# Kernel tuning notes

Measured on AMD Instinct MI355X. Metric: run time of the kernel, lower is better.

## Reference

```python
import jax, jax.numpy as jnp
import numpy as np

EMBED = 1024
HEADS = 16
HEAD_DIM = EMBED // HEADS


def setup_inputs() -> dict:
    key = jax.random.key(0)
    ks = jax.random.split(key, 9)
    s = 1.0 / np.sqrt(EMBED)
    inp = {
        "x": jax.random.normal(ks[0], (2, 2048, EMBED), dtype=jnp.float32),
        "wq": jax.random.uniform(ks[1], (EMBED, EMBED), jnp.float32, -s, s),
        "bq": jax.random.uniform(ks[2], (EMBED,), jnp.float32, -s, s),
        "wk": jax.random.uniform(ks[3], (EMBED, EMBED), jnp.float32, -s, s),
        "bk": jax.random.uniform(ks[4], (EMBED,), jnp.float32, -s, s),
        "wv": jax.random.uniform(ks[5], (EMBED, EMBED), jnp.float32, -s, s),
        "bv": jax.random.uniform(ks[6], (EMBED,), jnp.float32, -s, s),
        "wo": jax.random.uniform(ks[7], (EMBED, EMBED), jnp.float32, -s, s),
        "bo": jax.random.uniform(ks[8], (EMBED,), jnp.float32, -s, s),
    }
    return inp


def reference(x, wq, bq, wk, bk, wv, bv, wo, bo):
    B, S, E = x.shape
    H, D = HEADS, HEAD_DIM
    # projections (torch Linear: y = x @ W.T + b; here weights stored as [E, E] applied as x @ W.T)
    q = (x @ wq.T + bq).reshape(B, S, H, D).transpose(0, 2, 1, 3)  # [B,H,S,D]
    k = (x @ wk.T + bk).reshape(B, S, H, D).transpose(0, 2, 1, 3)
    v = (x @ wv.T + bv).reshape(B, S, H, D).transpose(0, 2, 1, 3)
    scores = jnp.einsum("bhqd,bhkd->bhqk", q, k) / jnp.sqrt(jnp.asarray(D, x.dtype))
    attn = jax.nn.softmax(scores, axis=-1)  # dropout is identity in eval / p=0
    ctx = jnp.einsum("bhqk,bhkd->bhqd", attn, v)
    ctx = ctx.transpose(0, 2, 1, 3).reshape(B, S, E)
    return ctx @ wo.T + bo
```

## Files before the change

kernel.cpp:

```cpp
#include <hip/hip_runtime.h>
#include <hip/hip_bf16.h>

#define EMBED 1024
#define HEADS 16
#define HDIM  64
#define BATCH 2
#define SEQ   2048
#define MTOT  (BATCH*SEQ)

typedef __attribute__((ext_vector_type(8))) short bf16x8;
typedef __attribute__((ext_vector_type(4))) short bf16x4;
typedef __attribute__((ext_vector_type(4))) float f32x4;
typedef __attribute__((ext_vector_type(8))) unsigned short u16x8;
typedef __attribute__((ext_vector_type(2))) unsigned u32x2;
typedef __attribute__((ext_vector_type(4))) unsigned u32x4;

__device__ __forceinline__ unsigned pack2(float lo, float hi) {
    __hip_bfloat162 h = __float22bfloat162_rn(make_float2(lo, hi));
    unsigned u;
    __builtin_memcpy(&u, &h, sizeof(u));
    return u;
}
__device__ __forceinline__ unsigned short f2bf(float f) {
    __hip_bfloat16 h = __float2bfloat16(f);
    unsigned short u;
    __builtin_memcpy(&u, &h, sizeof(u));
    return u;
}
__device__ __forceinline__ u16x8 cvt8(float4 a, float4 b) {
    u32x4 r;
    r[0] = pack2(a.x, a.y);
    r[1] = pack2(a.z, a.w);
    r[2] = pack2(b.x, b.y);
    r[3] = pack2(b.z, b.w);
    return __builtin_bit_cast(u16x8, r);
}

__device__ __forceinline__ f32x4 mfma16(bf16x4 a, bf16x4 b, f32x4 c) {
#if __has_builtin(__builtin_amdgcn_mfma_f32_16x16x16bf16_1k)
    return __builtin_amdgcn_mfma_f32_16x16x16bf16_1k(a, b, c, 0, 0, 0);
#else
    f32x4 d;
    asm volatile("v_mfma_f32_16x16x16_bf16 %0, %1, %2, %3"
                 : "=v"(d) : "v"(a), "v"(b), "v"(c));
    return d;
#endif
}

__global__ __launch_bounds__(256, 2) void qkv_proj(
    const float* __restrict__ x,
    const float* __restrict__ wq, const float* __restrict__ bq,
    const float* __restrict__ wk, const float* __restrict__ bk,
    const float* __restrict__ wv, const float* __restrict__ bv,
    unsigned short* __restrict__ qo,
    unsigned short* __restrict__ ko,
    unsigned short* __restrict__ vto)
{
    const int which = blockIdx.z;
    const float* __restrict__ w    = (which == 0) ? wq : (which == 1) ? wk : wv;
    const float* __restrict__ bias = (which == 0) ? bq : (which == 1) ? bk : bv;
    const float kscale = (which == 1) ? 0.18033688f : 1.0f;

    const int m0 = blockIdx.x * 128;
    const int n0 = blockIdx.y * 128;

    __shared__ unsigned short a_lds[128][40];
    __shared__ unsigned short b_lds[128][40];

    const int tid  = threadIdx.x;
    const int lane = tid & 63;
    const int wid  = tid >> 6;
    const int wr   = wid >> 1, wc = wid & 1;
    const int lq   = lane & 15;
    const int lg   = lane >> 4;

    f32x4 acc[4][4] = {};

    const int srow = tid >> 2;
    const int scol = (tid & 3) * 8;

    for (int k0 = 0; k0 < EMBED; k0 += 32) {
        #pragma unroll
        for (int p = 0; p < 2; ++p) {
            const int r = srow + p * 64;
            const float4* sa = (const float4*)(x + (size_t)(m0 + r) * EMBED + k0 + scol);
            *(u16x8*)&a_lds[r][scol] = cvt8(sa[0], sa[1]);
            const float4* sb = (const float4*)(w + (size_t)(n0 + r) * EMBED + k0 + scol);
            *(u16x8*)&b_lds[r][scol] = cvt8(sb[0], sb[1]);
        }
        __syncthreads();
        bf16x8 af[4], bfr[4];
        #pragma unroll
        for (int i = 0; i < 4; ++i)
            af[i] = *(const bf16x8*)&a_lds[wr*64 + i*16 + lq][lg*8];
        #pragma unroll
        for (int j = 0; j < 4; ++j)
            bfr[j] = *(const bf16x8*)&b_lds[wc*64 + j*16 + lq][lg*8];
        #pragma unroll
        for (int i = 0; i < 4; ++i)
            #pragma unroll
            for (int j = 0; j < 4; ++j)
                acc[i][j] = __builtin_amdgcn_mfma_f32_16x16x32_bf16(af[i], bfr[j], acc[i][j], 0, 0, 0);
        __syncthreads();
    }

    #pragma unroll
    for (int j = 0; j < 4; ++j) {
        const int nn = n0 + wc*64 + j*16 + lq;
        const float bsv = bias[nn];
        const int h = nn >> 6, d = nn & (HDIM-1);
        #pragma unroll
        for (int i = 0; i < 4; ++i) {
            const int mmb = m0 + wr*64 + i*16 + lg*4;
            const int b = mmb >> 11;
            const int s = mmb & (SEQ-1);
            const size_t bh = (size_t)(b*HEADS + h);
            if (which == 2) {
                u32x2 ov;
                ov[0] = pack2(acc[i][j][0] + bsv, acc[i][j][1] + bsv);
                ov[1] = pack2(acc[i][j][2] + bsv, acc[i][j][3] + bsv);
                *(u32x2*)&vto[(bh*HDIM + d)*SEQ + s] = ov;
            } else {
                unsigned short* o = (which == 0) ? qo : ko;
                #pragma unroll
                for (int r = 0; r < 4; ++r)
                    o[(bh*SEQ + (s + r))*HDIM + d] = f2bf((acc[i][j][r] + bsv) * kscale);
            }
        }
    }
}

__global__ __launch_bounds__(256, 4) void attn(
    const unsigned short* __restrict__ q,
    const unsigned short* __restrict__ k,
    const unsigned short* __restrict__ vt,
    unsigned short* __restrict__ ctx)
{
    __shared__ __align__(16) unsigned char sm[2 * 16384];

    const int bid   = blockIdx.x;
    const int xcd   = bid & 7;
    const int local = bid >> 3;
    const int bh    = xcd * 4 + (local >> 5);
    const int q0    = (local & 31) * 64;
    const int b     = bh >> 4;
    const int h     = bh & (HEADS - 1);
    const int tid   = threadIdx.x;
    const int wv    = tid >> 6;
    const int lane  = tid & 63;
    const int lq = lane & 15, lg = lane >> 4;

    const unsigned short* qb = q  + (size_t)bh * SEQ * HDIM;
    const unsigned short* kb = k  + (size_t)bh * SEQ * HDIM;
    const unsigned short* vb = vt + (size_t)bh * HDIM * SEQ;

    const int swz    = (lq & 7) << 4;
    const int kread0 = lq*128 + ((lg*16)      ^ swz);
    const int kread1 = lq*128 + ((lg*16 + 64) ^ swz);
    int vroff[4];
    #pragma unroll
    for (int sub = 0; sub < 4; ++sub)
        vroff[sub] = lq*128 + ((sub*32 + lg*8) ^ swz);

    const int wrow = tid >> 3;
    const int woff = wrow*128 + ((((tid & 7) * 16)) ^ ((wrow & 7) << 4));

    const int scol = (tid & 7) * 8;
    const unsigned short* kp = kb + (size_t)wrow * HDIM + scol;
    const unsigned short* vp = vb + (size_t)wrow * SEQ + scol;

    bf16x8 qf[2];
    #pragma unroll
    for (int hh = 0; hh < 2; ++hh)
        qf[hh] = *(const bf16x8*)(qb + (size_t)(q0 + wv*16 + lq) * HDIM + hh*32 + lg*8);

    f32x4 o[4] = {};
    float lr = 0.f;

    u16x8 kr0, kr1, vr0, vr1;

#define LOADT() do {                                                           \
    kr0 = *(const u16x8*)(kp);                                                 \
    kr1 = *(const u16x8*)(kp + 32*HDIM);                                       \
    vr0 = *(const u16x8*)(vp);                                                 \
    vr1 = *(const u16x8*)(vp + 32*SEQ);                                        \
} while (0)

#define WRITET(BF) do {                                                        \
    *(u16x8*)(sm + (BF)*16384 +         woff) = kr0;                           \
    *(u16x8*)(sm + (BF)*16384 +  4096 + woff) = kr1;                           \
    *(u16x8*)(sm + (BF)*16384 +  8192 + woff) = vr0;                           \
    *(u16x8*)(sm + (BF)*16384 + 12288 + woff) = vr1;                           \
} while (0)

#define COMPUTE(BF) do {                                                       \
    f32x4 s_[4];                                                               \
    _Pragma("unroll")                                                          \
    for (int sub = 0; sub < 4; ++sub) {                                        \
        bf16x8 k0 = *(const bf16x8*)(sm + (BF)*16384 + sub*2048 + kread0);     \
        bf16x8 k1 = *(const bf16x8*)(sm + (BF)*16384 + sub*2048 + kread1);     \
        f32x4 z = {};                                                          \
        z = __builtin_amdgcn_mfma_f32_16x16x32_bf16(k0, qf[0], z, 0, 0, 0);    \
        z = __builtin_amdgcn_mfma_f32_16x16x32_bf16(k1, qf[1], z, 0, 0, 0);    \
        s_[sub] = z;                                                           \
    }                                                                          \
    bf16x4 pf[4];                                                              \
    float psum = 0.f;                                                          \
    _Pragma("unroll")                                                          \
    for (int sub = 0; sub < 4; ++sub) {                                        \
        f32x4 pv;                                                              \
        _Pragma("unroll")                                                      \
        for (int r = 0; r < 4; ++r) pv[r] = exp2f(s_[sub][r]);                 \
        psum += (pv[0] + pv[1]) + (pv[2] + pv[3]);                             \
        u32x2 pk;                                                              \
        pk[0] = pack2(pv[0], pv[1]);                                           \
        pk[1] = pack2(pv[2], pv[3]);                                           \
        pf[sub] = __builtin_bit_cast(bf16x4, pk);                              \
    }                                                                          \
    lr += psum;                                                                \
    _Pragma("unroll")                                                          \
    for (int sub = 0; sub < 4; ++sub) {                                        \
        _Pragma("unroll")                                                      \
        for (int i = 0; i < 4; ++i) {                                          \
            bf16x4 vfr = *(const bf16x4*)(sm + (BF)*16384 + 8192 + i*2048      \
                                          + vroff[sub]);                       \
            o[i] = mfma16(vfr, pf[sub], o[i]);                                 \
        }                                                                      \
    }                                                                          \
} while (0)

    LOADT();
    WRITET(0);
    __syncthreads();
    kp += 64 * HDIM;
    vp += 64;

    for (int t2 = 0; t2 < 16; ++t2) {
        {
            const int t = 2 * t2;
            if (t < 31) LOADT();
            COMPUTE(0);
            if (t < 31) {
                WRITET(1);
                __syncthreads();
                kp += 64 * HDIM;
                vp += 64;
            }
        }
        {
            const int t = 2 * t2 + 1;
            if (t < 31) LOADT();
            COMPUTE(1);
            if (t < 31) {
                WRITET(0);
                __syncthreads();
                kp += 64 * HDIM;
                vp += 64;
            }
        }
    }

#undef LOADT
#undef WRITET
#undef COMPUTE

    float lm = lr + __shfl_xor(lr, 16);
    lm += __shfl_xor(lm, 32);
    const float inv = 1.0f / lm;
    unsigned short* cb = ctx + ((size_t)(b*SEQ + q0 + wv*16 + lq)) * EMBED + h*HDIM;
    #pragma unroll
    for (int i = 0; i < 4; ++i) {
        u32x2 ov;
        ov[0] = pack2(o[i][0] * inv, o[i][1] * inv);
        ov[1] = pack2(o[i][2] * inv, o[i][3] * inv);
        *(u32x2*)(cb + i*16 + lg*4) = ov;
    }
}

__global__ __launch_bounds__(256, 2) void out_proj(
    const unsigned short* __restrict__ ctx,
    const float* __restrict__ wo, const float* __restrict__ bo,
    float* __restrict__ out)
{
    const int m0 = blockIdx.x * 128;
    const int n0 = blockIdx.y * 128;

    __shared__ unsigned short a_lds[128][40];
    __shared__ unsigned short b_lds[128][40];

    const int tid  = threadIdx.x;
    const int lane = tid & 63;
    const int wid  = tid >> 6;
    const int wr   = wid >> 1, wc = wid & 1;
    const int lq   = lane & 15;
    const int lg   = lane >> 4;

    f32x4 acc[4][4] = {};

    const int srow = tid >> 2;
    const int scol = (tid & 3) * 8;

    for (int k0 = 0; k0 < EMBED; k0 += 32) {
        #pragma unroll
        for (int p = 0; p < 2; ++p) {
            const int r = srow + p * 64;
            *(u16x8*)&a_lds[r][scol] =
                *(const u16x8*)(ctx + (size_t)(m0 + r) * EMBED + k0 + scol);
            const float4* sb = (const float4*)(wo + (size_t)(n0 + r) * EMBED + k0 + scol);
            *(u16x8*)&b_lds[r][scol] = cvt8(sb[0], sb[1]);
        }
        __syncthreads();
        bf16x8 af[4], bfr[4];
        #pragma unroll
        for (int i = 0; i < 4; ++i)
            af[i] = *(const bf16x8*)&a_lds[wr*64 + i*16 + lq][lg*8];
        #pragma unroll
        for (int j = 0; j < 4; ++j)
            bfr[j] = *(const bf16x8*)&b_lds[wc*64 + j*16 + lq][lg*8];
        #pragma unroll
        for (int i = 0; i < 4; ++i)
            #pragma unroll
            for (int j = 0; j < 4; ++j)
                acc[i][j] = __builtin_amdgcn_mfma_f32_16x16x32_bf16(af[i], bfr[j], acc[i][j], 0, 0, 0);
        __syncthreads();
    }

    #pragma unroll
    for (int j = 0; j < 4; ++j) {
        const int nn = n0 + wc*64 + j*16 + lq;
        const float bsv = bo[nn];
        #pragma unroll
        for (int i = 0; i < 4; ++i) {
            const int mm = m0 + wr*64 + i*16 + lg*4;
            #pragma unroll
            for (int r = 0; r < 4; ++r)
                out[(size_t)(mm + r) * EMBED + nn] = acc[i][j][r] + bsv;
        }
    }
}

extern "C" void kernel_launch(void* const* d_in, const int* in_sizes, int n_in,
                              void* d_out, int out_size, void* d_ws, size_t ws_size,
                              hipStream_t stream) {
    const float* x  = (const float*)d_in[0];
    const float* wq = (const float*)d_in[1];
    const float* bq = (const float*)d_in[2];
    const float* wk = (const float*)d_in[3];
    const float* bk = (const float*)d_in[4];
    const float* wv = (const float*)d_in[5];
    const float* bv = (const float*)d_in[6];
    const float* wo = (const float*)d_in[7];
    const float* bo = (const float*)d_in[8];
    float* out = (float*)d_out;

    const size_t NELEM = (size_t)MTOT * EMBED;
    unsigned short* q_ws   = (unsigned short*)d_ws;
    unsigned short* k_ws   = q_ws  + NELEM;
    unsigned short* vt_ws  = k_ws  + NELEM;
    unsigned short* ctx_ws = vt_ws + NELEM;

    qkv_proj<<<dim3(MTOT/128, EMBED/128, 3), 256, 0, stream>>>(
        x, wq, bq, wk, bk, wv, bv, q_ws, k_ws, vt_ws);
    attn<<<dim3(SEQ/64 * BATCH*HEADS), 256, 0, stream>>>(q_ws, k_ws, vt_ws, ctx_ws);
    out_proj<<<dim3(MTOT/128, EMBED/128), 256, 0, stream>>>(ctx_ws, wo, bo, out);
}
```

Baseline: 150.9 us.

## Load V fragments directly from global memory into registers, bypassing LDS

The attention kernel now has each wave read its V^T MFMA operand fragments straight from global memory into registers at the start of each tile, instead of staging V through shared memory. This halves the LDS footprint and removes the V LDS stores and reads. In exchange, every wave in the block re-reads the same V data from global memory or cache with narrow 8-byte loads. The loads are issued right before the compute that consumes them, so their latency may be exposed and register pressure rises.

```diff
diff --git a/kernel.cpp b/kernel.cpp
--- a/kernel.cpp
+++ b/kernel.cpp
@@ -136,7 +136,7 @@
     const unsigned short* __restrict__ vt,
     unsigned short* __restrict__ ctx)
 {
-    __shared__ __align__(16) unsigned char sm[2 * 16384];
+    __shared__ __align__(16) unsigned char sm[2 * 8192];
 
     const int bid   = blockIdx.x;
     const int xcd   = bid & 7;
@@ -157,17 +157,17 @@
     const int swz    = (lq & 7) << 4;
     const int kread0 = lq*128 + ((lg*16)      ^ swz);
     const int kread1 = lq*128 + ((lg*16 + 64) ^ swz);
-    int vroff[4];
-    #pragma unroll
-    for (int sub = 0; sub < 4; ++sub)
-        vroff[sub] = lq*128 + ((sub*32 + lg*8) ^ swz);
 
     const int wrow = tid >> 3;
     const int woff = wrow*128 + ((((tid & 7) * 16)) ^ ((wrow & 7) << 4));
 
     const int scol = (tid & 7) * 8;
     const unsigned short* kp = kb + (size_t)wrow * HDIM + scol;
-    const unsigned short* vp = vb + (size_t)wrow * SEQ + scol;
+
+    const unsigned short* vbp[4];
+    #pragma unroll
+    for (int i = 0; i < 4; ++i)
+        vbp[i] = vb + (size_t)(i*16 + lq) * SEQ + lg*4;
 
     bf16x8 qf[2];
     #pragma unroll
@@ -177,28 +177,36 @@
     f32x4 o[4] = {};
     float lr = 0.f;
 
-    u16x8 kr0, kr1, vr0, vr1;
+    u16x8 kr0, kr1;
+    bf16x4 vf[4][4];
 
 #define LOADT() do {                                                           \
     kr0 = *(const u16x8*)(kp);                                                 \
     kr1 = *(const u16x8*)(kp + 32*HDIM);                                       \
-    vr0 = *(const u16x8*)(vp);                                                 \
-    vr1 = *(const u16x8*)(vp + 32*SEQ);                                        \
 } while (0)
 
 #define WRITET(BF) do {                                                        \
-    *(u16x8*)(sm + (BF)*16384 +         woff) = kr0;                           \
-    *(u16x8*)(sm + (BF)*16384 +  4096 + woff) = kr1;                           \
-    *(u16x8*)(sm + (BF)*16384 +  8192 + woff) = vr0;                           \
-    *(u16x8*)(sm + (BF)*16384 + 12288 + woff) = vr1;                           \
+    *(u16x8*)(sm + (BF)*8192 +        woff) = kr0;                             \
+    *(u16x8*)(sm + (BF)*8192 + 4096 + woff) = kr1;                             \
+} while (0)
+
+#define VISSUE() do {                                                          \
+    _Pragma("unroll")                                                          \
+    for (int i = 0; i < 4; ++i) {                                              \
+        vf[0][i] = *(const bf16x4*)(vbp[i]);                                   \
+        vf[1][i] = *(const bf16x4*)(vbp[i] + 16);                              \
+        vf[2][i] = *(const bf16x4*)(vbp[i] + 32);                              \
+        vf[3][i] = *(const bf16x4*)(vbp[i] + 48);                              \
+        vbp[i] += 64;                                                          \
+    }                                                                          \
 } while (0)
 
 #define COMPUTE(BF) do {                                                       \
     f32x4 s_[4];                                                               \
     _Pragma("unroll")                                                          \
     for (int sub = 0; sub < 4; ++sub) {                                        \
-        bf16x8 k0 = *(const bf16x8*)(sm + (BF)*16384 + sub*2048 + kread0);     \
-        bf16x8 k1 = *(const bf16x8*)(sm + (BF)*16384 + sub*2048 + kread1);     \
+        bf16x8 k0 = *(const bf16x8*)(sm + (BF)*8192 + sub*2048 + kread0);      \
+        bf16x8 k1 = *(const bf16x8*)(sm + (BF)*8192 + sub*2048 + kread1);      \
         f32x4 z = {};                                                          \
         z = __builtin_amdgcn_mfma_f32_16x16x32_bf16(k0, qf[0], z, 0, 0, 0);    \
         z = __builtin_amdgcn_mfma_f32_16x16x32_bf16(k1, qf[1], z, 0, 0, 0);    \
@@ -221,11 +229,8 @@
     _Pragma("unroll")                                                          \
     for (int sub = 0; sub < 4; ++sub) {                                        \
         _Pragma("unroll")                                                      \
-        for (int i = 0; i < 4; ++i) {                                          \
-            bf16x4 vfr = *(const bf16x4*)(sm + (BF)*16384 + 8192 + i*2048      \
-                                          + vroff[sub]);                       \
-            o[i] = mfma16(vfr, pf[sub], o[i]);                                 \
-        }                                                                      \
+        for (int i = 0; i < 4; ++i)                                            \
+            o[i] = mfma16(vf[sub][i], pf[sub], o[i]);                          \
     }                                                                          \
 } while (0)
 
@@ -233,35 +238,35 @@
     WRITET(0);
     __syncthreads();
     kp += 64 * HDIM;
-    vp += 64;
 
     for (int t2 = 0; t2 < 16; ++t2) {
         {
             const int t = 2 * t2;
+            VISSUE();
             if (t < 31) LOADT();
             COMPUTE(0);
             if (t < 31) {
                 WRITET(1);
                 __syncthreads();
                 kp += 64 * HDIM;
-                vp += 64;
             }
         }
         {
             const int t = 2 * t2 + 1;
+            VISSUE();
             if (t < 31) LOADT();
             COMPUTE(1);
             if (t < 31) {
                 WRITET(0);
                 __syncthreads();
                 kp += 64 * HDIM;
-                vp += 64;
             }
         }
     }
 
 #undef LOADT
 #undef WRITET
+#undef VISSUE
 #undef COMPUTE
 
     float lm = lr + __shfl_xor(lr, 16);
```

Measured after the change: 334.5 us. 122% more time.
